# Performance work log

Measured on AMD Instinct MI355X. Metric: run time of the kernel, lower is better.

The kernel has to match this reference:

```python
import jax, jax.numpy as jnp
import numpy as np

B, C, H, W = 16, 256, 64, 64
NH, WS = 8, 8  # num_heads, window_size
HD = C // NH   # head_dim = 32


def setup_inputs() -> dict:
    key = jax.random.key(0)
    k1, k2, k3 = jax.random.split(key, 3)
    x = jax.random.normal(k1, (B, C, H, W), dtype=jnp.float32)
    w_qkv = jax.random.normal(k2, (3 * C, C), dtype=jnp.float32) * 0.02  # 1x1 conv, no bias
    w_proj = jax.random.normal(k3, (C, C), dtype=jnp.float32) * 0.02
    return {"x": x, "w_qkv": w_qkv, "w_proj": w_proj, "shift": 1}


def _window_partition(t, ws):
    # [b,c,h,w] -> [b*(h/ws)*(w/ws), ws*ws, c]
    b, c, h, w = t.shape
    t = t.reshape(b, c, h // ws, ws, w // ws, ws)
    t = t.transpose(0, 2, 4, 3, 5, 1)
    return t.reshape(-1, ws * ws, c)


def _window_reverse(t, b, c, h, w, ws):
    t = t.reshape(b, h // ws, w // ws, ws, ws, c)
    t = t.transpose(0, 5, 1, 3, 2, 4)
    return t.reshape(b, c, h, w)


def reference(x, w_qkv, w_proj, shift):
    b, c, h, w = x.shape
    ws = min(WS, h, w)
    shift_size = ws // 2 if (shift and ws > 1 and h % ws == 0 and w % ws == 0) else 0
    if shift_size > 0:
        x = jnp.roll(x, (-shift_size, -shift_size), axis=(2, 3))
    # 1x1 conv QKV: [b,c,h,w] x [3c,c] -> [b,3c,h,w]
    qkv = jnp.einsum('bchw,oc->bohw', x, w_qkv)
    q, k, v = jnp.split(qkv, 3, axis=1)
    q_t = _window_partition(q, ws)  # [Bw, S, c], S = ws*ws
    k_t = _window_partition(k, ws)
    v_t = _window_partition(v, ws)
    bw, s, _ = q_t.shape
    # heads: [Bw, nh, S, hd]
    qh = q_t.reshape(bw, s, NH, HD).transpose(0, 2, 1, 3)
    kh = k_t.reshape(bw, s, NH, HD).transpose(0, 2, 1, 3)
    vh = v_t.reshape(bw, s, NH, HD).transpose(0, 2, 1, 3)
    scale = 1.0 / jnp.sqrt(jnp.asarray(HD, dtype=qh.dtype))
    scores = jnp.einsum('bnqd,bnkd->bnqk', qh, kh) * scale
    attn = jax.nn.softmax(scores, axis=-1)
    out = jnp.einsum('bnqk,bnkd->bnqd', attn, vh)
    out = out.transpose(0, 2, 1, 3).reshape(bw, s, c)
    out = _window_reverse(out, b, c, h, w, ws)
    if shift_size > 0:
        out = jnp.roll(out, (shift_size, shift_size), axis=(2, 3))
    return jnp.einsum('bchw,oc->bohw', out, w_proj)
```

## Files before the change

kernel.cpp:

```cpp
#include <hip/hip_runtime.h>

typedef short bf16x8 __attribute__((ext_vector_type(8)));
typedef float f32x4 __attribute__((ext_vector_type(4)));
typedef unsigned short u16;
typedef unsigned int u32;

static __device__ __forceinline__ u16 f2bf(float f) {
  u32 u = __builtin_bit_cast(u32, f);
  u32 r = (u + 0x7FFFu + ((u >> 16) & 1u)) >> 16;
  return (u16)r;
}

__global__ __launch_bounds__(256) void k_conv(
    const float* __restrict__ wqkv, const float* __restrict__ wproj,
    u16* __restrict__ wbf) {
  const int cid = blockIdx.x * 256 + threadIdx.x;
  const float* src;
  int dst;
  if (cid < 24576) {
    const int tile = cid >> 9, rem = cid & 511;
    const int k = rem >> 6, lane = rem & 63;
    src = wqkv + (size_t)(tile * 16 + (lane & 15)) * 256 + k * 32 + (lane >> 4) * 8;
    dst = cid;
  } else {
    const int pid = cid - 24576;
    const int mt = pid >> 9, rem = pid & 511;
    const int h = rem >> 6, lane = rem & 63;
    src = wproj + (size_t)(mt * 16 + (lane & 15)) * 256 + h * 32 + (lane >> 4) * 8;
    dst = 24576 + h * 1024 + mt * 64 + lane;
  }
  float4 f0 = *(const float4*)(src);
  float4 f1 = *(const float4*)(src + 4);
  ushort4 a, b;
  a.x = f2bf(f0.x); a.y = f2bf(f0.y); a.z = f2bf(f0.z); a.w = f2bf(f0.w);
  b.x = f2bf(f1.x); b.y = f2bf(f1.y); b.z = f2bf(f1.z); b.w = f2bf(f1.w);
  *(ushort4*)(wbf + (size_t)dst * 8) = a;
  *(ushort4*)(wbf + (size_t)dst * 8 + 4) = b;
}

#define B0 0
#define B1 4096
#define B2 8192
#define B3 12288
#define QH 16384
#define KH 18944
#define VTH 21504
#define PH 23808
#define LDS_TOT 28416

#define MEMF() asm volatile("" ::: "memory")
#define BAR()                        \
  do {                               \
    MEMF();                          \
    __builtin_amdgcn_s_barrier();    \
    MEMF();                          \
  } while (0)
#define ENTRY()                                                      \
  do {                                                               \
    asm volatile("s_waitcnt vmcnt(0) lgkmcnt(0)" ::: "memory");      \
    __builtin_amdgcn_s_barrier();                                    \
    MEMF();                                                          \
  } while (0)
#define WLG0() asm volatile("s_waitcnt lgkmcnt(0)" ::: "memory")

#define GL2LDS(gp, lp)                                   \
  __builtin_amdgcn_global_load_lds(                      \
      (__attribute__((address_space(1))) void*)(gp),     \
      (__attribute__((address_space(3))) void*)(lp), 16, 0, 0)

static __device__ __forceinline__ void stage_half(const u16* g, u16* l, int t) {
#pragma unroll
  for (int j = 0; j < 2; ++j) {
    const int off = (j * 256 + t) * 8;
    GL2LDS(g + off, l + off);
  }
}

#define GEMM_TILE(BUFB, DSTB, U)                                              \
  do {                                                                        \
    const u16* wb_ = LDS + (BUFB) + lane * 8;                                 \
    f32x4 a0 = {0.f, 0.f, 0.f, 0.f}, a1 = {0.f, 0.f, 0.f, 0.f};               \
    _Pragma("unroll") for (int k = 0; k < 8; ++k) {                           \
      const bf16x8 bf_ = *(const bf16x8*)(wb_ + k * 512);                     \
      a0 = __builtin_amdgcn_mfma_f32_16x16x32_bf16(af0[k], bf_, a0, 0, 0, 0); \
      a1 = __builtin_amdgcn_mfma_f32_16x16x32_bf16(af1[k], bf_, a1, 0, 0, 0); \
    }                                                                         \
    _Pragma("unroll") for (int r = 0; r < 4; ++r) {                           \
      LDS[(DSTB) + (wp * 32 + quad * 4 + r) * 40 + (U) * 16 + l15] =          \
          f2bf(a0[r]);                                                        \
      LDS[(DSTB) + (wp * 32 + 16 + quad * 4 + r) * 40 + (U) * 16 + l15] =     \
          f2bf(a1[r]);                                                        \
    }                                                                         \
  } while (0)

#define VGEMM_TILE(BUFB, U)                                                   \
  do {                                                                        \
    const u16* wb_ = LDS + (BUFB) + lane * 8;                                 \
    f32x4 a0 = {0.f, 0.f, 0.f, 0.f}, a1 = {0.f, 0.f, 0.f, 0.f};               \
    _Pragma("unroll") for (int k = 0; k < 8; ++k) {                           \
      const bf16x8 bf_ = *(const bf16x8*)(wb_ + k * 512);                     \
      a0 = __builtin_amdgcn_mfma_f32_16x16x32_bf16(af0[k], bf_, a0, 0, 0, 0); \
      a1 = __builtin_amdgcn_mfma_f32_16x16x32_bf16(af1[k], bf_, a1, 0, 0, 0); \
    }                                                                         \
    ushort4 pk0, pk1;                                                         \
    pk0.x = f2bf(a0[0]); pk0.y = f2bf(a0[1]);                                 \
    pk0.z = f2bf(a0[2]); pk0.w = f2bf(a0[3]);                                 \
    pk1.x = f2bf(a1[0]); pk1.y = f2bf(a1[1]);                                 \
    pk1.z = f2bf(a1[2]); pk1.w = f2bf(a1[3]);                                 \
    *(ushort4*)&LDS[VTH + ((U) * 16 + l15) * 72 + wp * 32 + quad * 4] = pk0;  \
    *(ushort4*)&LDS[VTH + ((U) * 16 + l15) * 72 + wp * 32 + 16 + quad * 4] =  \
        pk1;                                                                  \
  } while (0)

__global__ __launch_bounds__(256, 2) void k_fused(
    const float* __restrict__ x, const u16* __restrict__ wbf,
    const int* __restrict__ shiftp, float* __restrict__ out) {
  __shared__ u16 LDS[LDS_TOT];
  const int blk = blockIdx.x;
  const int win = ((blk & 127) << 3) | (blk >> 7);
  const int b = win >> 6, wh = (win >> 3) & 7, ww = win & 7;
  const int off = (shiftp[0] != 0) ? 4 : 0;
  const int t = threadIdx.x;

  {
    const int slot = (blk >> 8) & 3;
    if (slot == 1) __builtin_amdgcn_s_sleep(16);
    else if (slot == 2) __builtin_amdgcn_s_sleep(32);
    else if (slot == 3) __builtin_amdgcn_s_sleep(48);
  }

  {
    u16* X = LDS;
    const int wr = t & 7;
    const int h = ((wh << 3) + wr + off) & 63;
    const int w0 = ((ww << 3) + off) & 63;
    const int w1 = ((ww << 3) + off + 4) & 63;
    const int p0 = wr << 3;
#pragma unroll
    for (int it = 0; it < 8; ++it) {
      const int c = (t >> 3) + (it << 5);
      const float* src = x + ((size_t)(b * 256 + c) * 64 + h) * 64;
      float4 v0 = *(const float4*)(src + w0);
      float4 v1 = *(const float4*)(src + w1);
      X[(p0 + 0) * 264 + c] = f2bf(v0.x);
      X[(p0 + 1) * 264 + c] = f2bf(v0.y);
      X[(p0 + 2) * 264 + c] = f2bf(v0.z);
      X[(p0 + 3) * 264 + c] = f2bf(v0.w);
      X[(p0 + 4) * 264 + c] = f2bf(v1.x);
      X[(p0 + 5) * 264 + c] = f2bf(v1.y);
      X[(p0 + 6) * 264 + c] = f2bf(v1.z);
      X[(p0 + 7) * 264 + c] = f2bf(v1.w);
    }
  }
  __syncthreads();

  const int lane = t & 63, wv = t >> 6;
  const int l15 = lane & 15, quad = lane >> 4;
  const int wp = wv >> 1, wc = wv & 1;
  const int apos0 = wv * 16 + quad * 4;

  bf16x8 af0[8], af1[8];
#pragma unroll
  for (int k = 0; k < 8; ++k) {
    af0[k] = *(const bf16x8*)&LDS[(wp * 32 + l15) * 264 + quad * 8 + k * 32];
    af1[k] =
        *(const bf16x8*)&LDS[(wp * 32 + 16 + l15) * 264 + quad * 8 + k * 32];
  }
  WLG0();
  BAR();

  stage_half(wbf, LDS + B0, t);
  stage_half(wbf + (size_t)17 * 4096, LDS + B1, t);

  f32x4 accP[8][2];
#pragma unroll
  for (int mt = 0; mt < 8; ++mt) {
    accP[mt][0] = (f32x4){0.f, 0.f, 0.f, 0.f};
    accP[mt][1] = (f32x4){0.f, 0.f, 0.f, 0.f};
  }

  const float scale = 0.17677669529663687f;
  u16* Pw = LDS + PH + wv * 1152;

#pragma unroll 1
  for (int h = 0; h < 8; ++h) {
    ENTRY();
    stage_half(wbf + (size_t)(h * 2 + 1) * 4096, LDS + B2, t);
    stage_half(wbf + (size_t)(32 + h * 2) * 4096, LDS + B3, t);
    if (wc == 0) GEMM_TILE(B0, QH, 0);
    else GEMM_TILE(B1, KH, 1);
    ENTRY();
    stage_half(wbf + (size_t)(16 + h * 2) * 4096, LDS + B0, t);
    stage_half(wbf + (size_t)(33 + h * 2) * 4096, LDS + B1, t);
    if (wc == 0) GEMM_TILE(B2, QH, 1);
    else VGEMM_TILE(B3, 0);
    ENTRY();
    stage_half(wbf + 196608 + (size_t)h * 8192, LDS + B2, t);
    stage_half(wbf + 196608 + (size_t)h * 8192 + 4096, LDS + B3, t);
    if (wc == 0) GEMM_TILE(B0, KH, 0);
    else VGEMM_TILE(B1, 1);
    ENTRY();
    if (h < 7) {
      stage_half(wbf + (size_t)((h + 1) * 2) * 4096, LDS + B0, t);
      stage_half(wbf + (size_t)(17 + (h + 1) * 2) * 4096, LDS + B1, t);
    }
    {
      bf16x8 aq = *(const bf16x8*)&LDS[QH + (wv * 16 + l15) * 40 + quad * 8];
      f32x4 sc[4];
#pragma unroll
      for (int nt = 0; nt < 4; ++nt) {
        bf16x8 bk = *(const bf16x8*)&LDS[KH + (nt * 16 + l15) * 40 + quad * 8];
        f32x4 z = {0.f, 0.f, 0.f, 0.f};
        sc[nt] = __builtin_amdgcn_mfma_f32_16x16x32_bf16(aq, bk, z, 0, 0, 0);
      }
#pragma unroll
      for (int r = 0; r < 4; ++r) {
        float mx = -1e30f;
#pragma unroll
        for (int nt = 0; nt < 4; ++nt) mx = fmaxf(mx, sc[nt][r]);
        mx = fmaxf(mx, __shfl_xor(mx, 1));
        mx = fmaxf(mx, __shfl_xor(mx, 2));
        mx = fmaxf(mx, __shfl_xor(mx, 4));
        mx = fmaxf(mx, __shfl_xor(mx, 8));
        float p[4], sum = 0.f;
#pragma unroll
        for (int nt = 0; nt < 4; ++nt) {
          p[nt] = __expf((sc[nt][r] - mx) * scale);
          sum += p[nt];
        }
        sum += __shfl_xor(sum, 1);
        sum += __shfl_xor(sum, 2);
        sum += __shfl_xor(sum, 4);
        sum += __shfl_xor(sum, 8);
        const float is = 1.f / sum;
#pragma unroll
        for (int nt = 0; nt < 4; ++nt)
          Pw[(quad * 4 + r) * 72 + nt * 16 + l15] = f2bf(p[nt] * is);
      }
      f32x4 oa[2];
      oa[0] = (f32x4){0.f, 0.f, 0.f, 0.f};
      oa[1] = (f32x4){0.f, 0.f, 0.f, 0.f};
#pragma unroll
      for (int kk = 0; kk < 2; ++kk) {
        bf16x8 ap = *(const bf16x8*)&Pw[l15 * 72 + kk * 32 + quad * 8];
#pragma unroll
        for (int n2 = 0; n2 < 2; ++n2) {
          bf16x8 bv = *(const bf16x8*)&LDS[VTH + (n2 * 16 + l15) * 72 +
                                           kk * 32 + quad * 8];
          oa[n2] = __builtin_amdgcn_mfma_f32_16x16x32_bf16(ap, bv, oa[n2], 0, 0, 0);
        }
      }
#pragma unroll
      for (int n2 = 0; n2 < 2; ++n2)
#pragma unroll
        for (int r = 0; r < 4; ++r)
          LDS[QH + (apos0 + r) * 40 + n2 * 16 + l15] = f2bf(oa[n2][r]);
    }
    WLG0();
    BAR();
    {
      const int pjb = (wc == 0) ? B2 : B3;
      bf16x8 bo0 =
          *(const bf16x8*)&LDS[QH + (wp * 32 + l15) * 40 + quad * 8];
      bf16x8 bo1 =
          *(const bf16x8*)&LDS[QH + (wp * 32 + 16 + l15) * 40 + quad * 8];
#pragma unroll
      for (int mt = 0; mt < 8; ++mt) {
        bf16x8 aw = *(const bf16x8*)&LDS[pjb + mt * 512 + lane * 8];
        accP[mt][0] =
            __builtin_amdgcn_mfma_f32_16x16x32_bf16(aw, bo0, accP[mt][0], 0, 0, 0);
        accP[mt][1] =
            __builtin_amdgcn_mfma_f32_16x16x32_bf16(aw, bo1, accP[mt][1], 0, 0, 0);
      }
    }
  }

#pragma unroll
  for (int i = 0; i < 2; ++i) {
    const int pos = wp * 32 + i * 16 + l15;
    const int hco = ((wh << 3) + (pos >> 3) + off) & 63;
    const int wco = ((ww << 3) + (pos & 7) + off) & 63;
#pragma unroll
    for (int mt = 0; mt < 8; ++mt)
#pragma unroll
      for (int r = 0; r < 4; ++r) {
        const int c = wc * 128 + mt * 16 + quad * 4 + r;
        out[((size_t)(b * 256 + c) << 12) + (hco << 6) + wco] = accP[mt][i][r];
      }
  }
}

extern "C" void kernel_launch(void* const* d_in, const int* in_sizes, int n_in,
                              void* d_out, int out_size, void* d_ws, size_t ws_size,
                              hipStream_t stream) {
  const float* x = (const float*)d_in[0];
  const float* wqkv = (const float*)d_in[1];
  const float* wproj = (const float*)d_in[2];
  const int* shiftp = (const int*)d_in[3];
  float* outp = (float*)d_out;
  u16* wbf = (u16*)d_ws;
  hipLaunchKernelGGL(k_conv, dim3(128), dim3(256), 0, stream, wqkv, wproj, wbf);
  hipLaunchKernelGGL(k_fused, dim3(1024), dim3(256), 0, stream, x, wbf, shiftp, outp);
}
```

Measured before the change: 221.6 us.

## Load weight fragments directly from global into registers instead of LDS staging

Drops the double-buffered global-to-LDS staging of the QKV and projection weight tiles, along with the four full barriers per head. Each wave now loads its bf16 weight MFMA fragments straight from global memory (L2-resident) into registers. This shrinks LDS use from about 57KB to about 34KB, which could let more blocks fit per CU. In exchange it raises VGPR pressure, issues more global loads (weights are no longer shared across waves through LDS), exposes load latency without explicit prefetch, and adds a barrier at the end of each head iteration.

```diff
diff --git a/kernel.cpp b/kernel.cpp
--- a/kernel.cpp
+++ b/kernel.cpp
@@ -38,15 +38,11 @@
   *(ushort4*)(wbf + (size_t)dst * 8 + 4) = b;
 }
 
-#define B0 0
-#define B1 4096
-#define B2 8192
-#define B3 12288
-#define QH 16384
-#define KH 18944
-#define VTH 21504
-#define PH 23808
-#define LDS_TOT 28416
+#define QH 0
+#define KH 2560
+#define VTH 5120
+#define PH 7424
+#define LDS_TOT 16896
 
 #define MEMF() asm volatile("" ::: "memory")
 #define BAR()                        \
@@ -55,35 +51,21 @@
     __builtin_amdgcn_s_barrier();    \
     MEMF();                          \
   } while (0)
-#define ENTRY()                                                      \
-  do {                                                               \
-    asm volatile("s_waitcnt vmcnt(0) lgkmcnt(0)" ::: "memory");      \
-    __builtin_amdgcn_s_barrier();                                    \
-    MEMF();                                                          \
-  } while (0)
 #define WLG0() asm volatile("s_waitcnt lgkmcnt(0)" ::: "memory")
 
-#define GL2LDS(gp, lp)                                   \
-  __builtin_amdgcn_global_load_lds(                      \
-      (__attribute__((address_space(1))) void*)(gp),     \
-      (__attribute__((address_space(3))) void*)(lp), 16, 0, 0)
-
-static __device__ __forceinline__ void stage_half(const u16* g, u16* l, int t) {
-#pragma unroll
-  for (int j = 0; j < 2; ++j) {
-    const int off = (j * 256 + t) * 8;
-    GL2LDS(g + off, l + off);
-  }
-}
-
-#define GEMM_TILE(BUFB, DSTB, U)                                              \
+#define LOADF(FR, TI)                                              \
+  do {                                                             \
+    const u16* fp_ = wbf + (size_t)(TI) * 4096 + lane * 8;         \
+    _Pragma("unroll") for (int k = 0; k < 8; ++k)                  \
+        FR[k] = *(const bf16x8*)(fp_ + k * 512);                   \
+  } while (0)
+
+#define GEMM_TILE_F(FR, DSTB, U)                                              \
   do {                                                                        \
-    const u16* wb_ = LDS + (BUFB) + lane * 8;                                 \
     f32x4 a0 = {0.f, 0.f, 0.f, 0.f}, a1 = {0.f, 0.f, 0.f, 0.f};               \
     _Pragma("unroll") for (int k = 0; k < 8; ++k) {                           \
-      const bf16x8 bf_ = *(const bf16x8*)(wb_ + k * 512);                     \
-      a0 = __builtin_amdgcn_mfma_f32_16x16x32_bf16(af0[k], bf_, a0, 0, 0, 0); \
-      a1 = __builtin_amdgcn_mfma_f32_16x16x32_bf16(af1[k], bf_, a1, 0, 0, 0); \
+      a0 = __builtin_amdgcn_mfma_f32_16x16x32_bf16(af0[k], FR[k], a0, 0, 0, 0);\
+      a1 = __builtin_amdgcn_mfma_f32_16x16x32_bf16(af1[k], FR[k], a1, 0, 0, 0);\
     }                                                                         \
     _Pragma("unroll") for (int r = 0; r < 4; ++r) {                           \
       LDS[(DSTB) + (wp * 32 + quad * 4 + r) * 40 + (U) * 16 + l15] =          \
@@ -93,14 +75,12 @@
     }                                                                         \
   } while (0)
 
-#define VGEMM_TILE(BUFB, U)                                                   \
+#define V_TILE_F(FR, U)                                                       \
   do {                                                                        \
-    const u16* wb_ = LDS + (BUFB) + lane * 8;                                 \
     f32x4 a0 = {0.f, 0.f, 0.f, 0.f}, a1 = {0.f, 0.f, 0.f, 0.f};               \
     _Pragma("unroll") for (int k = 0; k < 8; ++k) {                           \
-      const bf16x8 bf_ = *(const bf16x8*)(wb_ + k * 512);                     \
-      a0 = __builtin_amdgcn_mfma_f32_16x16x32_bf16(af0[k], bf_, a0, 0, 0, 0); \
-      a1 = __builtin_amdgcn_mfma_f32_16x16x32_bf16(af1[k], bf_, a1, 0, 0, 0); \
+      a0 = __builtin_amdgcn_mfma_f32_16x16x32_bf16(af0[k], FR[k], a0, 0, 0, 0);\
+      a1 = __builtin_amdgcn_mfma_f32_16x16x32_bf16(af1[k], FR[k], a1, 0, 0, 0);\
     }                                                                         \
     ushort4 pk0, pk1;                                                         \
     pk0.x = f2bf(a0[0]); pk0.y = f2bf(a0[1]);                                 \
@@ -169,9 +149,6 @@
   WLG0();
   BAR();
 
-  stage_half(wbf, LDS + B0, t);
-  stage_half(wbf + (size_t)17 * 4096, LDS + B1, t);
-
   f32x4 accP[8][2];
 #pragma unroll
   for (int mt = 0; mt < 8; ++mt) {
@@ -184,26 +161,20 @@
 
 #pragma unroll 1
   for (int h = 0; h < 8; ++h) {
-    ENTRY();
-    stage_half(wbf + (size_t)(h * 2 + 1) * 4096, LDS + B2, t);
-    stage_half(wbf + (size_t)(32 + h * 2) * 4096, LDS + B3, t);
-    if (wc == 0) GEMM_TILE(B0, QH, 0);
-    else GEMM_TILE(B1, KH, 1);
-    ENTRY();
-    stage_half(wbf + (size_t)(16 + h * 2) * 4096, LDS + B0, t);
-    stage_half(wbf + (size_t)(33 + h * 2) * 4096, LDS + B1, t);
-    if (wc == 0) GEMM_TILE(B2, QH, 1);
-    else VGEMM_TILE(B3, 0);
-    ENTRY();
-    stage_half(wbf + 196608 + (size_t)h * 8192, LDS + B2, t);
-    stage_half(wbf + 196608 + (size_t)h * 8192 + 4096, LDS + B3, t);
-    if (wc == 0) GEMM_TILE(B0, KH, 0);
-    else VGEMM_TILE(B1, 1);
-    ENTRY();
-    if (h < 7) {
-      stage_half(wbf + (size_t)((h + 1) * 2) * 4096, LDS + B0, t);
-      stage_half(wbf + (size_t)(17 + (h + 1) * 2) * 4096, LDS + B1, t);
-    }
+    {
+      bf16x8 fA[8], fB[8];
+      const int t0 = wc ? (17 + h * 2) : (h * 2);
+      const int t1 = wc ? (32 + h * 2) : (h * 2 + 1);
+      const int t2 = wc ? (33 + h * 2) : (16 + h * 2);
+      LOADF(fA, t0);
+      LOADF(fB, t1);
+      if (wc == 0) GEMM_TILE_F(fA, QH, 0); else GEMM_TILE_F(fA, KH, 1);
+      LOADF(fA, t2);
+      if (wc == 0) GEMM_TILE_F(fB, QH, 1); else V_TILE_F(fB, 0);
+      if (wc == 0) GEMM_TILE_F(fA, KH, 0); else V_TILE_F(fA, 1);
+    }
+    WLG0();
+    BAR();
     {
       bf16x8 aq = *(const bf16x8*)&LDS[QH + (wv * 16 + l15) * 40 + quad * 8];
       f32x4 sc[4];
@@ -256,23 +227,29 @@
         for (int r = 0; r < 4; ++r)
           LDS[QH + (apos0 + r) * 40 + n2 * 16 + l15] = f2bf(oa[n2][r]);
     }
+    bf16x8 pjf[8];
+    {
+      const u16* pp_ =
+          wbf + 196608 + (size_t)h * 8192 + (size_t)wc * 4096 + lane * 8;
+#pragma unroll
+      for (int j = 0; j < 8; ++j) pjf[j] = *(const bf16x8*)(pp_ + j * 512);
+    }
     WLG0();
     BAR();
     {
-      const int pjb = (wc == 0) ? B2 : B3;
-      bf16x8 bo0 =
-          *(const bf16x8*)&LDS[QH + (wp * 32 + l15) * 40 + quad * 8];
+      bf16x8 bo0 = *(const bf16x8*)&LDS[QH + (wp * 32 + l15) * 40 + quad * 8];
       bf16x8 bo1 =
           *(const bf16x8*)&LDS[QH + (wp * 32 + 16 + l15) * 40 + quad * 8];
 #pragma unroll
       for (int mt = 0; mt < 8; ++mt) {
-        bf16x8 aw = *(const bf16x8*)&LDS[pjb + mt * 512 + lane * 8];
         accP[mt][0] =
-            __builtin_amdgcn_mfma_f32_16x16x32_bf16(aw, bo0, accP[mt][0], 0, 0, 0);
+            __builtin_amdgcn_mfma_f32_16x16x32_bf16(pjf[mt], bo0, accP[mt][0], 0, 0, 0);
         accP[mt][1] =
-            __builtin_amdgcn_mfma_f32_16x16x32_bf16(aw, bo1, accP[mt][1], 0, 0, 0);
-      }
-    }
+            __builtin_amdgcn_mfma_f32_16x16x32_bf16(pjf[mt], bo1, accP[mt][1], 0, 0, 0);
+      }
+    }
+    WLG0();
+    BAR();
   }
 
 #pragma unroll
```

After: 211.7 us. 4.4% less time.
